# Optimization experiments

Hardware: AMD Instinct MI355X
Metric: run time of the kernel (lower is better)

## Reference

```python
import jax, jax.numpy as jnp
import numpy as np

B, C, H, W, NMAX = 16, 1, 128, 8192, 64


def setup_inputs() -> dict:
    key = jax.random.key(0)
    x = jax.random.normal(key, (B, C, H, W), dtype=jnp.float32)
    # Build realistic non-overlapping, sorted chirp boundaries with numpy.
    rng = np.random.default_rng(0)
    slot = W // NMAX  # 128 columns per chirp slot
    gaps = rng.integers(0, 40, size=(B, NMAX))
    widths = rng.integers(20, slot - 40, size=(B, NMAX))
    starts = np.arange(NMAX)[None, :] * slot + gaps
    ends = starts + widths
    n = rng.integers(48, NMAX + 1, size=(B,)).astype(np.int32)
    xi = np.stack([starts, ends], axis=-1).astype(np.int32)
    valid = np.arange(NMAX)[None, :] < n[:, None]
    xi = xi * valid[:, :, None]  # zero out invalid rows
    return {
        "x": x,
        "xi": jnp.asarray(xi),
        "N": jnp.asarray(n),
        "sep_param": jnp.zeros((1, 1, 1), dtype=jnp.float32),  # learned sep token scalar
    }


def reference(x, xi, N, sep_param):
    """Vectorized TinyBird.compactify_data: remove silence between chirp
    blocks, packing blocks contiguously with 1-column separators.
    Returns (x_new, xi_new). x_new keeps full width W (original truncates
    to data-dependent w_max; padding beyond w_max is zeros, same values)."""
    Bb, Cc, Hh, Ww = x.shape
    nmax = xi.shape[1]
    idx = jnp.arange(nmax, dtype=jnp.int32)[None, :]            # (1, Nmax)
    Nc = N.reshape(Bb, 1).astype(jnp.int32)                      # (B, 1)
    w = jnp.clip(xi[:, :, 1] - xi[:, :, 0], 0, None).astype(jnp.int32)
    valid = idx < Nc                                             # (B, Nmax)
    wv = jnp.where(valid, w, 0)
    csum = jnp.cumsum(wv, axis=1)
    start_new = csum - wv + idx                                  # compressed starts
    end_new = csum + idx                                         # compressed ends
    xi_new = jnp.where(valid[:, :, None],
                       jnp.stack([start_new, end_new], axis=-1), 0).astype(xi.dtype)

    # For every output column j, find which compressed segment it falls in.
    j = jnp.arange(Ww, dtype=jnp.int32)
    big = jnp.int32(Ww + nmax + 2)
    start_search = jnp.where(valid, start_new, big)              # keep sorted
    seg = jax.vmap(lambda s: jnp.searchsorted(s, j, side='right'))(start_search) - 1
    seg = jnp.clip(seg, 0, nmax - 1)                             # (B, W)
    bidx = jnp.arange(Bb)[:, None]
    s_new = start_new[bidx, seg]
    e_new = end_new[bidx, seg]
    seg_valid = valid[bidx, seg]
    in_seg = seg_valid & (j[None, :] >= s_new) & (j[None, :] < e_new)
    is_sep = seg_valid & (j[None, :] == e_new) & (seg < (Nc - 1))
    src = jnp.clip(xi[bidx, seg, 0].astype(jnp.int32) + (j[None, :] - s_new), 0, Ww - 1)
    src_full = jnp.broadcast_to(src[:, None, None, :], (Bb, Cc, Hh, Ww))
    gathered = jnp.take_along_axis(x, src_full, axis=3)          # ragged gather
    sep_val = sep_param[0, 0, 0]                                 # sep_token column value
    x_new = jnp.where(in_seg[:, None, None, :], gathered,
                      jnp.where(is_sep[:, None, None, :], sep_val, jnp.float32(0)))
    return x_new, xi_new
```

## Files before the change

### kernel.cpp

```cpp
#include <hip/hip_runtime.h>

#define Bn 16
#define Hn 128
#define Wn 8192
#define NMAX 64

typedef float nt_f4 __attribute__((ext_vector_type(4)));

__global__ __launch_bounds__(256) void row_pack_lds_kernel(
    const float* __restrict__ x, const int* __restrict__ xi,
    const int* __restrict__ N, const float* __restrict__ sep_param,
    float* __restrict__ out, float* __restrict__ out_xi) {
    __shared__ float s_row[Wn];
    __shared__ int s_start[NMAX];
    __shared__ int s_w[NMAX];
    __shared__ int s_src0[NMAX];
    __shared__ int s_n, s_tail, s_wide;

    const int row = blockIdx.x;
    const int b   = row >> 7;
    const int tid = threadIdx.x;

    if (tid < NMAX) {
        int nb = N[b];
        int s0 = xi[(b * NMAX + tid) * 2 + 0];
        int s1 = xi[(b * NMAX + tid) * 2 + 1];
        int w = s1 - s0; if (w < 0) w = 0;
        bool valid = tid < nb;
        int wv = valid ? w : 0;
        int c = wv;
        #pragma unroll
        for (int d = 1; d < 64; d <<= 1) {
            int t = __shfl_up(c, d, 64);
            if (tid >= d) c += t;
        }
        int start_new = c - wv + tid;
        int end_new   = c + tid;
        s_start[tid] = start_new;
        s_w[tid]     = wv;
        s_src0[tid]  = s0;
        unsigned long long wide = __ballot(wv > 127);
        if (tid == 0) {
            s_n = nb;
            s_wide = (wide != 0ULL) ? 1 : 0;
        }
        int last = (nb > 0) ? (nb - 1) : 0;
        if (tid == last) s_tail = (nb > 0) ? end_new : 0;
        if ((row & 127) == 0) {
            out_xi[(b * NMAX + tid) * 2 + 0] = valid ? (float)start_new : 0.0f;
            out_xi[(b * NMAX + tid) * 2 + 1] = valid ? (float)end_new : 0.0f;
        }
    }
    __syncthreads();

    const int nb   = s_n;
    const int tail = s_tail;
    const float sep = sep_param[0];
    const float* __restrict__ xrow = x + (size_t)row * Wn;
    float* __restrict__ orow = out + (size_t)row * Wn;
    const int wave = tid >> 6;
    const int lane = tid & 63;

    float v0[16], v1[16];
    int sg_s[16], sg_wt[16];
    #pragma unroll
    for (int k = 0; k < 16; ++k) {
        const int seg = wave + 4 * k;
        const bool act = seg < nb;
        const int s    = act ? s_start[seg] : 0;
        const int w    = act ? s_w[seg] : 0;
        const int src0 = act ? s_src0[seg] : 0;
        sg_s[k]  = s;
        sg_wt[k] = act ? (w + ((seg < nb - 1) ? 1 : 0)) : 0;
        v0[k] = (lane < w)      ? xrow[src0 + lane]      : sep;
        v1[k] = (lane + 64 < w) ? xrow[src0 + lane + 64] : sep;
    }

    #pragma unroll
    for (int k = 0; k < 16; ++k) {
        if (lane < sg_wt[k])      s_row[sg_s[k] + lane]      = v0[k];
        if (lane + 64 < sg_wt[k]) s_row[sg_s[k] + lane + 64] = v1[k];
    }

    if (s_wide) {
        for (int seg = wave; seg < nb; seg += 4) {
            const int w = s_w[seg];
            const int wtot = w + ((seg < nb - 1) ? 1 : 0);
            for (int l = 128 + lane; l < wtot; l += 64) {
                s_row[s_start[seg] + l] = (l < w) ? xrow[s_src0[seg] + l] : sep;
            }
        }
    }

    const int t4 = (tail + 3) & ~3;
    if (tid < (t4 - tail)) s_row[tail + tid] = 0.0f;
    float4* s_row4 = reinterpret_cast<float4*>(s_row);
    const float4 z4 = make_float4(0.0f, 0.0f, 0.0f, 0.0f);
    for (int i4 = (t4 >> 2) + tid; i4 < (Wn >> 2); i4 += 256) {
        s_row4[i4] = z4;
    }
    __syncthreads();

    nt_f4* orow4 = reinterpret_cast<nt_f4*>(orow);
    #pragma unroll
    for (int g = 0; g < 8; ++g) {
        float4 t = s_row4[g * 256 + tid];
        nt_f4 v = {t.x, t.y, t.z, t.w};
        __builtin_nontemporal_store(v, orow4 + g * 256 + tid);
    }
}

extern "C" void kernel_launch(void* const* d_in, const int* in_sizes, int n_in,
                              void* d_out, int out_size, void* d_ws, size_t ws_size,
                              hipStream_t stream) {
    const float* x   = (const float*)d_in[0];
    const int* xi    = (const int*)d_in[1];
    const int* N     = (const int*)d_in[2];
    const float* sep = (const float*)d_in[3];

    float* out_x  = (float*)d_out;
    float* out_xi = (float*)d_out + (size_t)Bn * Hn * Wn;

    row_pack_lds_kernel<<<Bn * Hn, 256, 0, stream>>>(x, xi, N, sep, out_x, out_xi);
}
```

Before: 116.4 us.

## Replace per-row LDS packing with per-segment column-rectangle copy and separate zero-fill blocks

The kernel no longer assigns one block per row and stages the whole row in LDS. Each block now copies one segment across all 128 rows of a batch with scalar loads and nontemporal scalar stores, and separate blocks zero-fill the tail region of each row. This removes the LDS staging and the block-wide barriers, and it only writes the zero region past the packed data. In exchange the data copies become scalar 4-byte accesses with short, possibly misaligned column runs per row instead of float4 stores. The grid also shrinks to 96 blocks per batch.

```diff
diff --git a/kernel.cpp b/kernel.cpp
--- a/kernel.cpp
+++ b/kernel.cpp
@@ -5,108 +5,90 @@
 #define Wn 8192
 #define NMAX 64
 
+#define SEG_BLKS 64
+#define ZERO_BLKS 32
+#define BLKS_PER_B (SEG_BLKS + ZERO_BLKS)
+#define ROWS_PER_ZB (Hn / ZERO_BLKS)
+
 typedef float nt_f4 __attribute__((ext_vector_type(4)));
 
-__global__ __launch_bounds__(256) void row_pack_lds_kernel(
+__global__ __launch_bounds__(256) void pack_rect_kernel(
     const float* __restrict__ x, const int* __restrict__ xi,
     const int* __restrict__ N, const float* __restrict__ sep_param,
     float* __restrict__ out, float* __restrict__ out_xi) {
-    __shared__ float s_row[Wn];
-    __shared__ int s_start[NMAX];
-    __shared__ int s_w[NMAX];
-    __shared__ int s_src0[NMAX];
-    __shared__ int s_n, s_tail, s_wide;
+    const int b    = blockIdx.y;
+    const int k    = blockIdx.x;
+    const int tid  = threadIdx.x;
+    const int lane = tid & 63;
+    const int wave = tid >> 6;
 
-    const int row = blockIdx.x;
-    const int b   = row >> 7;
-    const int tid = threadIdx.x;
+    const int nb = N[b];
+    const int s0 = xi[(b * NMAX + lane) * 2 + 0];
+    const int s1 = xi[(b * NMAX + lane) * 2 + 1];
+    int w = s1 - s0; if (w < 0) w = 0;
+    const bool valid = lane < nb;
+    const int wv = valid ? w : 0;
+    int c = wv;
+    #pragma unroll
+    for (int d = 1; d < 64; d <<= 1) {
+        int t = __shfl_up(c, d, 64);
+        if (lane >= d) c += t;
+    }
+    const int start_new = c - wv + lane;
+    const int end_new   = c + lane;
 
-    if (tid < NMAX) {
-        int nb = N[b];
-        int s0 = xi[(b * NMAX + tid) * 2 + 0];
-        int s1 = xi[(b * NMAX + tid) * 2 + 1];
-        int w = s1 - s0; if (w < 0) w = 0;
-        bool valid = tid < nb;
-        int wv = valid ? w : 0;
-        int c = wv;
-        #pragma unroll
-        for (int d = 1; d < 64; d <<= 1) {
-            int t = __shfl_up(c, d, 64);
-            if (tid >= d) c += t;
-        }
-        int start_new = c - wv + tid;
-        int end_new   = c + tid;
-        s_start[tid] = start_new;
-        s_w[tid]     = wv;
-        s_src0[tid]  = s0;
-        unsigned long long wide = __ballot(wv > 127);
-        if (tid == 0) {
-            s_n = nb;
-            s_wide = (wide != 0ULL) ? 1 : 0;
-        }
-        int last = (nb > 0) ? (nb - 1) : 0;
-        if (tid == last) s_tail = (nb > 0) ? end_new : 0;
-        if ((row & 127) == 0) {
-            out_xi[(b * NMAX + tid) * 2 + 0] = valid ? (float)start_new : 0.0f;
-            out_xi[(b * NMAX + tid) * 2 + 1] = valid ? (float)end_new : 0.0f;
-        }
-    }
-    __syncthreads();
-
-    const int nb   = s_n;
-    const int tail = s_tail;
-    const float sep = sep_param[0];
-    const float* __restrict__ xrow = x + (size_t)row * Wn;
-    float* __restrict__ orow = out + (size_t)row * Wn;
-    const int wave = tid >> 6;
-    const int lane = tid & 63;
-
-    float v0[16], v1[16];
-    int sg_s[16], sg_wt[16];
-    #pragma unroll
-    for (int k = 0; k < 16; ++k) {
-        const int seg = wave + 4 * k;
-        const bool act = seg < nb;
-        const int s    = act ? s_start[seg] : 0;
-        const int w    = act ? s_w[seg] : 0;
-        const int src0 = act ? s_src0[seg] : 0;
-        sg_s[k]  = s;
-        sg_wt[k] = act ? (w + ((seg < nb - 1) ? 1 : 0)) : 0;
-        v0[k] = (lane < w)      ? xrow[src0 + lane]      : sep;
-        v1[k] = (lane + 64 < w) ? xrow[src0 + lane + 64] : sep;
+    if (k == 0 && wave == 0) {
+        out_xi[(b * NMAX + lane) * 2 + 0] = valid ? (float)start_new : 0.0f;
+        out_xi[(b * NMAX + lane) * 2 + 1] = valid ? (float)end_new   : 0.0f;
     }
 
-    #pragma unroll
-    for (int k = 0; k < 16; ++k) {
-        if (lane < sg_wt[k])      s_row[sg_s[k] + lane]      = v0[k];
-        if (lane + 64 < sg_wt[k]) s_row[sg_s[k] + lane + 64] = v1[k];
-    }
+    const float sep = sep_param[0];
+    float* __restrict__ ob = out + (size_t)b * Hn * Wn;
 
-    if (s_wide) {
-        for (int seg = wave; seg < nb; seg += 4) {
-            const int w = s_w[seg];
-            const int wtot = w + ((seg < nb - 1) ? 1 : 0);
-            for (int l = 128 + lane; l < wtot; l += 64) {
-                s_row[s_start[seg] + l] = (l < w) ? xrow[s_src0[seg] + l] : sep;
+    if (k < SEG_BLKS) {
+        const int seg = k;
+        if (seg >= nb) return;
+        const int seg_s = __shfl(start_new, seg);
+        const int seg_w = __shfl(wv, seg);
+        const int seg_a = __shfl(s0, seg);
+        const int wtot  = seg_w + ((seg < nb - 1) ? 1 : 0);
+        const float* __restrict__ xb = x + (size_t)b * Hn * Wn;
+
+        for (int c0 = 0; c0 < wtot; c0 += 64) {
+            const int col = c0 + lane;
+            if (col < wtot) {
+                const bool is_data = col < seg_w;
+                const int  src     = seg_a + col;
+                const int  dst     = seg_s + col;
+                for (int rr = 0; rr < 32; rr += 8) {
+                    float v[8];
+                    #pragma unroll
+                    for (int i = 0; i < 8; ++i) {
+                        const int r = wave + 4 * (rr + i);
+                        v[i] = is_data ? xb[(size_t)r * Wn + src] : sep;
+                    }
+                    #pragma unroll
+                    for (int i = 0; i < 8; ++i) {
+                        const int r = wave + 4 * (rr + i);
+                        __builtin_nontemporal_store(v[i], &ob[(size_t)r * Wn + dst]);
+                    }
+                }
             }
         }
-    }
-
-    const int t4 = (tail + 3) & ~3;
-    if (tid < (t4 - tail)) s_row[tail + tid] = 0.0f;
-    float4* s_row4 = reinterpret_cast<float4*>(s_row);
-    const float4 z4 = make_float4(0.0f, 0.0f, 0.0f, 0.0f);
-    for (int i4 = (t4 >> 2) + tid; i4 < (Wn >> 2); i4 += 256) {
-        s_row4[i4] = z4;
-    }
-    __syncthreads();
-
-    nt_f4* orow4 = reinterpret_cast<nt_f4*>(orow);
-    #pragma unroll
-    for (int g = 0; g < 8; ++g) {
-        float4 t = s_row4[g * 256 + tid];
-        nt_f4 v = {t.x, t.y, t.z, t.w};
-        __builtin_nontemporal_store(v, orow4 + g * 256 + tid);
+    } else {
+        const int tail = (nb > 0) ? __shfl(end_new, nb - 1) : 0;
+        const int t4   = (tail + 3) & ~3;
+        const int r0   = (k - SEG_BLKS) * ROWS_PER_ZB;
+        const nt_f4 z4 = {0.0f, 0.0f, 0.0f, 0.0f};
+        for (int r = r0; r < r0 + ROWS_PER_ZB; ++r) {
+            float* __restrict__ orow = ob + (size_t)r * Wn;
+            if (tid < (t4 - tail))
+                __builtin_nontemporal_store(0.0f, &orow[tail + tid]);
+            nt_f4* orow4 = reinterpret_cast<nt_f4*>(orow);
+            for (int i4 = (t4 >> 2) + tid; i4 < (Wn >> 2); i4 += 256) {
+                __builtin_nontemporal_store(z4, &orow4[i4]);
+            }
+        }
     }
 }
 
@@ -121,5 +103,6 @@
     float* out_x  = (float*)d_out;
     float* out_xi = (float*)d_out + (size_t)Bn * Hn * Wn;
 
-    row_pack_lds_kernel<<<Bn * Hn, 256, 0, stream>>>(x, xi, N, sep, out_x, out_xi);
+    dim3 grid(BLKS_PER_B, Bn);
+    pack_rect_kernel<<<grid, 256, 0, stream>>>(x, xi, N, sep, out_x, out_xi);
 }
```

Result: slower. 132.5 us (+13.9%).
